# Kernel tuning notes

Measured on AMD Instinct MI355X. Metric: run time of the kernel, lower is better.

Reference implementation:

```python
import jax, jax.numpy as jnp
import numpy as np

N_NODES = 50000
N_EDGES = 800000
D_IN, D_HID, D_OUT = 96, 96, 48


def _gcn_conv(x, src, dst, W, b, num_nodes):
    """PyG GCNConv: h = x @ W; out[dst] += norm * h[src]; out += b.
    Symmetric normalization deg^{-1/2}[src] * deg^{-1/2}[dst], self-loops included
    (src/dst already contain self-loops)."""
    h = x @ W  # [N, d_out]
    deg = jax.ops.segment_sum(jnp.ones_like(dst, dtype=h.dtype), dst,
                              num_segments=num_nodes)  # in-degree incl. self-loop
    dinv = jnp.where(deg > 0, jax.lax.rsqrt(deg), 0.0)
    norm = dinv[src] * dinv[dst]  # [E+N]
    msgs = h[src] * norm[:, None]  # gather + scale (the memory-bound part)
    out = jax.ops.segment_sum(msgs, dst, num_segments=num_nodes)  # scatter-add
    return out + b


def setup_inputs() -> dict:
    key = jax.random.key(0)
    k1, k2, k3, k4 = jax.random.split(key, 4)
    x = jax.random.normal(k1, (N_NODES, D_IN), dtype=jnp.float32)
    edge_index = jax.random.randint(k2, (2, N_EDGES), 0, N_NODES, dtype=jnp.int64)
    # Glorot-ish init for weights, zero bias (matches GCNConv defaults)
    W1 = jax.random.normal(k3, (D_IN, D_HID), dtype=jnp.float32) / np.sqrt(D_IN)
    b1 = jnp.zeros((D_HID,), dtype=jnp.float32)
    W2 = jax.random.normal(k4, (D_HID, D_OUT), dtype=jnp.float32) / np.sqrt(D_HID)
    b2 = jnp.zeros((D_OUT,), dtype=jnp.float32)
    return {"x": x, "edge_index": edge_index, "W1": W1, "b1": b1, "W2": W2, "b2": b2}


def reference(x, edge_index, W1, b1, W2, b2):
    num_nodes = x.shape[0]
    loops = jnp.arange(num_nodes, dtype=edge_index.dtype)
    src = jnp.concatenate([edge_index[0], loops])  # add self-loops
    dst = jnp.concatenate([edge_index[1], loops])
    h = _gcn_conv(x, src, dst, W1, b1, num_nodes)
    h = jax.nn.relu(h)
    # dropout p=0.5 is identity in eval mode (self.training=False)
    out = _gcn_conv(h, src, dst, W2, b2, num_nodes)
    return out
```

## Files before the change

### kernel.cpp

```cpp
#include <hip/hip_runtime.h>
#include <hip/hip_bf16.h>


constexpr int NN = 50000;
constexpr int NE = 800000;
constexpr int DI = 96;
constexpr int DH = 96;
constexpr int DO = 48;

constexpr int BK_SHIFT = 6;
constexpr int NBK      = (NN + 63) >> 6;
constexpr int BK_CAP   = 2048;

constexpr int NCHUNK = 128;
constexpr int CH     = (NE + NCHUNK - 1) / NCHUNK;

typedef unsigned short ushort8 __attribute__((ext_vector_type(8)));

__device__ __forceinline__ float bf2f(unsigned short u) {
    return __uint_as_float(((unsigned int)u) << 16);
}
__device__ __forceinline__ unsigned short f2bf(float f) {
    __hip_bfloat16 b = __float2bfloat16(f);
    return *reinterpret_cast<unsigned short*>(&b);
}


__global__ __launch_bounds__(256) void k_hist(const int* __restrict__ dst,
                                              int* __restrict__ C, int e) {
    __shared__ int hist[NBK];
    for (int i = threadIdx.x; i < NBK; i += 256) hist[i] = 0;
    __syncthreads();
    const int blk = blockIdx.x;
    const int beg = blk * CH, end = min(beg + CH, e);
    for (int i = beg + threadIdx.x; i < end; i += 256)
        atomicAdd(&hist[dst[i] >> BK_SHIFT], 1);
    __syncthreads();
    for (int b = threadIdx.x; b < NBK; b += 256)
        C[b * NCHUNK + blk] = hist[b];
}

__global__ __launch_bounds__(256) void k_rowscan(int* __restrict__ C,
                                                 int* __restrict__ totals,
                                                 int* __restrict__ row_ptr) {
    if (blockIdx.x == 0 && threadIdx.x == 0) row_ptr[NN] = NE;
    const int w    = threadIdx.x >> 6;
    const int lane = threadIdx.x & 63;
    const int r    = blockIdx.x * 4 + w;
    if (r >= NBK) return;
    int* row = C + r * NCHUNK;
    const int v0 = row[lane];
    const int v1 = row[64 + lane];
    int s0 = v0, s1 = v1;
#pragma unroll
    for (int off = 1; off < 64; off <<= 1) {
        int y0 = __shfl_up(s0, off);
        int y1 = __shfl_up(s1, off);
        if (lane >= off) { s0 += y0; s1 += y1; }
    }
    s1 += __shfl(s0, 63);
    row[lane]      = s0 - v0;
    row[64 + lane] = s1 - v1;
    if (lane == 63) totals[r] = s1;
}

__global__ __launch_bounds__(256) void k_scatter(const int* __restrict__ src,
                                                 const int* __restrict__ dst,
                                                 const int* __restrict__ C,
                                                 const int* __restrict__ totals,
                                                 int* __restrict__ bk_ptr,
                                                 unsigned* __restrict__ ebuf, int e) {
    __shared__ int bkL[NBK + 1];
    __shared__ int part[256];
    __shared__ int cur[NBK];
    const int t = threadIdx.x;

    int v[4];
    int s = 0;
    const int base = t * 4;
#pragma unroll
    for (int i = 0; i < 4; ++i) {
        int idx = base + i;
        v[i] = (idx < NBK) ? totals[idx] : 0;
        s += v[i];
    }
    part[t] = s;
    __syncthreads();
#pragma unroll
    for (int off = 1; off < 256; off <<= 1) {
        int x = part[t];
        int a = (t >= off) ? part[t - off] : 0;
        __syncthreads();
        part[t] = x + a;
        __syncthreads();
    }
    int run = part[t] - s;
#pragma unroll
    for (int i = 0; i < 4; ++i) {
        int idx = base + i;
        if (idx <= NBK) bkL[idx] = run;
        run += v[i];
    }
    __syncthreads();

    const int blk = blockIdx.x;
    for (int b = t; b < NBK; b += 256) cur[b] = bkL[b] + C[b * NCHUNK + blk];
    if (blk == 0)
        for (int i = t; i <= NBK; i += 256) bk_ptr[i] = bkL[i];
    __syncthreads();

    const int beg = blk * CH, end = min(beg + CH, e);
    for (int i = beg + t; i < end; i += 256) {
        int d = dst[i];
        int b = d >> BK_SHIFT;
        int pos = atomicAdd(&cur[b], 1);
        ebuf[pos] = ((unsigned)(d & 63) << 16) | (unsigned)src[i];
    }
}

__global__ __launch_bounds__(256) void k_bsort(const unsigned* __restrict__ ebuf,
                                               const int* __restrict__ bk_ptr,
                                               int* __restrict__ row_ptr,
                                               float* __restrict__ dinv,
                                               int* __restrict__ src_sorted, int n) {
    __shared__ unsigned eL[BK_CAP];
    __shared__ int outL[BK_CAP];
    __shared__ int curL[64];
    __shared__ int baseL[64];

    const int b   = blockIdx.x;
    const int beg = bk_ptr[b];
    const int m   = bk_ptr[b + 1] - beg;
    const int t   = threadIdx.x;

    if (t < 64) curL[t] = 0;
    __syncthreads();

    for (int i = t; i < m; i += 256) {
        unsigned v = ebuf[beg + i];
        eL[i] = v;
        atomicAdd(&curL[v >> 16], 1);
    }
    __syncthreads();

    if (t < 64) {
        int c = curL[t];
        int x = c;
#pragma unroll
        for (int off = 1; off < 64; off <<= 1) {
            int y = __shfl_up(x, off);
            if (t >= off) x += y;
        }
        int excl = x - c;
        baseL[t] = excl;
        int d0 = (b << BK_SHIFT) + t;
        if (d0 < n) {
            row_ptr[d0] = beg + excl;
            dinv[d0]    = rsqrtf((float)(c + 1));
        }
    }
    __syncthreads();
    if (t < 64) curL[t] = baseL[t];
    __syncthreads();

    for (int i = t; i < m; i += 256) {
        unsigned v = eL[i];
        int p = atomicAdd(&curL[v >> 16], 1);
        outL[p] = (int)(v & 0xFFFFu);
    }
    __syncthreads();
    for (int i = t; i < m; i += 256) src_sorted[beg + i] = outL[i];
}


template<int DOUT, bool XBF16>
__global__ __launch_bounds__(256) void k_gemm(const void* __restrict__ Xin,
                                              const float* __restrict__ W,
                                              const float* __restrict__ dinv,
                                              unsigned short* __restrict__ H, int n) {
    constexpr int ROWS = 32;
    constexpr int CPT  = DOUT / 16;
    constexpr int RPT  = 2;

    __shared__ float ws[DI * DOUT];
    __shared__ unsigned char xraw[ROWS * DI * (XBF16 ? 2 : 4)];
    float*          xsf = reinterpret_cast<float*>(xraw);
    unsigned short* xsu = reinterpret_cast<unsigned short*>(xraw);

    const int tid  = threadIdx.x;
    const int row0 = blockIdx.x * ROWS;

    for (int i = tid; i < DI * DOUT; i += 256) ws[i] = W[i];

    if (XBF16) {
        const ushort8* Xv = reinterpret_cast<const ushort8*>(
            (const unsigned short*)Xin + (size_t)row0 * DI);
        ushort8* xv = reinterpret_cast<ushort8*>(xsu);
        const int nv   = ROWS * DI / 8;
        const int maxv = ((n - row0) * DI) / 8;
        for (int i = tid; i < nv; i += 256)
            xv[i] = (i < maxv) ? Xv[i] : (ushort8)(0);
    } else {
        const float4* Xv = reinterpret_cast<const float4*>(
            (const float*)Xin + (size_t)row0 * DI);
        float4* xv = reinterpret_cast<float4*>(xsf);
        const int nv   = ROWS * DI / 4;
        const int maxv = ((n - row0) * DI) / 4;
        for (int i = tid; i < nv; i += 256)
            xv[i] = (i < maxv) ? Xv[i] : float4{0.f, 0.f, 0.f, 0.f};
    }
    __syncthreads();

    const int cg = tid & 15;
    const int rg = tid >> 4;

    float acc[RPT][CPT];
#pragma unroll
    for (int i = 0; i < RPT; ++i)
#pragma unroll
        for (int j = 0; j < CPT; ++j) acc[i][j] = 0.f;

    for (int k = 0; k < DI; ++k) {
        float xv[RPT];
#pragma unroll
        for (int i = 0; i < RPT; ++i) {
            int r = rg * RPT + i;
            xv[i] = XBF16 ? bf2f(xsu[r * DI + k]) : xsf[r * DI + k];
        }
#pragma unroll
        for (int j = 0; j < CPT; ++j) {
            float wv = ws[k * DOUT + cg * CPT + j];
#pragma unroll
            for (int i = 0; i < RPT; ++i) acc[i][j] += xv[i] * wv;
        }
    }

#pragma unroll
    for (int i = 0; i < RPT; ++i) {
        int row = row0 + rg * RPT + i;
        if (row < n) {
            float dv = dinv[row];
#pragma unroll
            for (int j = 0; j < CPT; ++j)
                H[(size_t)row * DOUT + cg * CPT + j] = f2bf(acc[i][j] * dv);
        }
    }
}


template<int D, bool RELU, bool OUTBF16>
__global__ __launch_bounds__(256) void k_agg_csr(const unsigned short* __restrict__ h,
                                                 const float* __restrict__ dinv,
                                                 const int* __restrict__ row_ptr,
                                                 const int* __restrict__ src_sorted,
                                                 const float* __restrict__ bias,
                                                 void* __restrict__ outp, int n) {
    constexpr int G = D / 8;
    int t = blockIdx.x * blockDim.x + threadIdx.x;
    if (t >= n * G) return;
    const int node = t / G;
    const int g    = t % G;

    const ushort8* h8 = reinterpret_cast<const ushort8*>(h);

    float accA[8], accB[8];
    {
        ushort8 hv = h8[(size_t)node * G + g];
#pragma unroll
        for (int j = 0; j < 8; ++j) { accA[j] = bf2f(hv[j]); accB[j] = 0.f; }
    }

    const int beg = row_ptr[node];
    const int end = row_ptr[node + 1];
    int k = beg;
    int kA = min((beg + 3) & ~3, end);
    for (; k < kA; ++k) {
        int s = src_sorted[k];
        ushort8 vv = h8[(size_t)s * G + g];
#pragma unroll
        for (int j = 0; j < 8; ++j) accA[j] += bf2f(vv[j]);
    }
    const int4* sv = reinterpret_cast<const int4*>(src_sorted + k);
    for (; k + 4 <= end; k += 4) {
        int4 s4 = *sv++;
        ushort8 v0 = h8[(size_t)s4.x * G + g];
        ushort8 v1 = h8[(size_t)s4.y * G + g];
        ushort8 v2 = h8[(size_t)s4.z * G + g];
        ushort8 v3 = h8[(size_t)s4.w * G + g];
#pragma unroll
        for (int j = 0; j < 8; ++j) {
            accA[j] += bf2f(v0[j]) + bf2f(v1[j]);
            accB[j] += bf2f(v2[j]) + bf2f(v3[j]);
        }
    }
    for (; k < end; ++k) {
        int s = src_sorted[k];
        ushort8 vv = h8[(size_t)s * G + g];
#pragma unroll
        for (int j = 0; j < 8; ++j) accA[j] += bf2f(vv[j]);
    }

    const float di = dinv[node];
    const float4* b4 = reinterpret_cast<const float4*>(bias);
    float4 b0 = b4[g * 2], b1 = b4[g * 2 + 1];
    float r[8];
#pragma unroll
    for (int j = 0; j < 8; ++j) r[j] = di * (accA[j] + accB[j]);
    r[0] += b0.x; r[1] += b0.y; r[2] += b0.z; r[3] += b0.w;
    r[4] += b1.x; r[5] += b1.y; r[6] += b1.z; r[7] += b1.w;
    if (RELU) {
#pragma unroll
        for (int j = 0; j < 8; ++j) r[j] = fmaxf(r[j], 0.f);
    }
    if (OUTBF16) {
        ushort8 o;
#pragma unroll
        for (int j = 0; j < 8; ++j) o[j] = f2bf(r[j]);
        reinterpret_cast<ushort8*>((unsigned short*)outp)[(size_t)node * G + g] = o;
    } else {
        float4* o4 = reinterpret_cast<float4*>((float*)outp + (size_t)node * D + g * 8);
        o4[0] = float4{r[0], r[1], r[2], r[3]};
        o4[1] = float4{r[4], r[5], r[6], r[7]};
    }
}


extern "C" void kernel_launch(void* const* d_in, const int* in_sizes, int n_in,
                              void* d_out, int out_size, void* d_ws, size_t ws_size,
                              hipStream_t stream) {
    const float* x   = (const float*)d_in[0];
    const int*   ei  = (const int*)d_in[1];
    const float* W1  = (const float*)d_in[2];
    const float* b1  = (const float*)d_in[3];
    const float* W2  = (const float*)d_in[4];
    const float* b2  = (const float*)d_in[5];
    float*       out = (float*)d_out;

    const int* srcv = ei;
    const int* dstv = ei + NE;

    char* p = (char*)d_ws;
    float*          dinv  = (float*)p;           p += (size_t)NN * 4;
    unsigned short* a1    = (unsigned short*)p;  p += (size_t)NN * DH * 2;
    unsigned short* h1    = (unsigned short*)p;  p += (size_t)NN * DH * 2;
    int*      row_ptr     = (int*)p;             p += (size_t)(NN + 16) * 4;
    int*      src_sorted  = (int*)p;             p += (size_t)NE * 4;
    unsigned* ebuf        = (unsigned*)p;        p += (size_t)NE * 4;
    int*      Cm          = (int*)p;             p += (size_t)NBK * NCHUNK * 4;
    int*      totals      = (int*)p;             p += (size_t)NBK * 4;
    int*      bk_ptr      = (int*)p;             p += (size_t)(NBK + 1) * 4;

    const int B = 256;

    k_hist<<<NCHUNK, B, 0, stream>>>(dstv, Cm, NE);
    k_rowscan<<<(NBK + 3) / 4, B, 0, stream>>>(Cm, totals, row_ptr);
    k_scatter<<<NCHUNK, B, 0, stream>>>(srcv, dstv, Cm, totals, bk_ptr, ebuf, NE);
    k_bsort<<<NBK, B, 0, stream>>>(ebuf, bk_ptr, row_ptr, dinv, src_sorted, NN);

    k_gemm<DH, false><<<(NN + 31) / 32, B, 0, stream>>>(x, W1, dinv, h1, NN);
    {
        int total = NN * (DH / 8);
        k_agg_csr<DH, true, true><<<(total + B - 1) / B, B, 0, stream>>>(
            h1, dinv, row_ptr, src_sorted, b1, a1, NN);
    }

    unsigned short* h2 = h1;
    k_gemm<DO, true><<<(NN + 31) / 32, B, 0, stream>>>(a1, W2, dinv, h2, NN);
    {
        int total = NN * (DO / 8);
        k_agg_csr<DO, false, false><<<(total + B - 1) / B, B, 0, stream>>>(
            h2, dinv, row_ptr, src_sorted, b2, out, NN);
    }
}
```

Before: 127.3 us.

## Slice node features into per-slice arrays and shrink source indices to 16-bit

Node feature matrices are stored as 8 column slices, each a separate padded array (16 bf16 for layer 1, 8 for layer 2). The aggregation kernels now run one thread per node per slice, so all gathers within a block hit one slice, which is small enough to stay cache-resident. Sorted source indices are stored as 16-bit values, halving index traffic. The costs are padding bytes, less coalesced output writes, and 16-bit indices only fit because the node count is below 65536.

```diff
diff --git a/kernel.cpp b/kernel.cpp
--- a/kernel.cpp
+++ b/kernel.cpp
@@ -15,7 +15,8 @@
 constexpr int NCHUNK = 128;
 constexpr int CH     = (NE + NCHUNK - 1) / NCHUNK;
 
-typedef unsigned short ushort8 __attribute__((ext_vector_type(8)));
+typedef unsigned short us4 __attribute__((ext_vector_type(4)));
+typedef unsigned short us8 __attribute__((ext_vector_type(8)));
 
 __device__ __forceinline__ float bf2f(unsigned short u) {
     return __uint_as_float(((unsigned int)u) << 16);
@@ -122,9 +123,9 @@
                                                const int* __restrict__ bk_ptr,
                                                int* __restrict__ row_ptr,
                                                float* __restrict__ dinv,
-                                               int* __restrict__ src_sorted, int n) {
+                                               unsigned short* __restrict__ src16, int n) {
     __shared__ unsigned eL[BK_CAP];
-    __shared__ int outL[BK_CAP];
+    __shared__ unsigned short outL[BK_CAP];
     __shared__ int curL[64];
     __shared__ int baseL[64];
 
@@ -166,161 +167,241 @@
     for (int i = t; i < m; i += 256) {
         unsigned v = eL[i];
         int p = atomicAdd(&curL[v >> 16], 1);
-        outL[p] = (int)(v & 0xFFFFu);
-    }
-    __syncthreads();
-    for (int i = t; i < m; i += 256) src_sorted[beg + i] = outL[i];
-}
-
-
-template<int DOUT, bool XBF16>
-__global__ __launch_bounds__(256) void k_gemm(const void* __restrict__ Xin,
-                                              const float* __restrict__ W,
-                                              const float* __restrict__ dinv,
-                                              unsigned short* __restrict__ H, int n) {
-    constexpr int ROWS = 32;
-    constexpr int CPT  = DOUT / 16;
-    constexpr int RPT  = 2;
-
-    __shared__ float ws[DI * DOUT];
-    __shared__ unsigned char xraw[ROWS * DI * (XBF16 ? 2 : 4)];
-    float*          xsf = reinterpret_cast<float*>(xraw);
-    unsigned short* xsu = reinterpret_cast<unsigned short*>(xraw);
+        outL[p] = (unsigned short)(v & 0xFFFFu);
+    }
+    __syncthreads();
+    for (int i = t; i < m; i += 256) src16[beg + i] = outL[i];
+}
+
+
+__global__ __launch_bounds__(256) void k_gemm1(const float* __restrict__ X,
+                                               const float* __restrict__ W,
+                                               const float* __restrict__ dinv,
+                                               unsigned short* __restrict__ Hsl, int n) {
+    __shared__ float ws[DI * DH];
+    __shared__ float xs[32 * DI];
+    unsigned short* hout = reinterpret_cast<unsigned short*>(xs);
 
     const int tid  = threadIdx.x;
-    const int row0 = blockIdx.x * ROWS;
-
-    for (int i = tid; i < DI * DOUT; i += 256) ws[i] = W[i];
-
-    if (XBF16) {
-        const ushort8* Xv = reinterpret_cast<const ushort8*>(
-            (const unsigned short*)Xin + (size_t)row0 * DI);
-        ushort8* xv = reinterpret_cast<ushort8*>(xsu);
-        const int nv   = ROWS * DI / 8;
-        const int maxv = ((n - row0) * DI) / 8;
-        for (int i = tid; i < nv; i += 256)
-            xv[i] = (i < maxv) ? Xv[i] : (ushort8)(0);
-    } else {
-        const float4* Xv = reinterpret_cast<const float4*>(
-            (const float*)Xin + (size_t)row0 * DI);
-        float4* xv = reinterpret_cast<float4*>(xsf);
-        const int nv   = ROWS * DI / 4;
+    const int row0 = blockIdx.x * 32;
+
+    for (int i = tid; i < DI * DH; i += 256) ws[i] = W[i];
+    {
+        const float4* Xv = reinterpret_cast<const float4*>(X + (size_t)row0 * DI);
+        float4* xv = reinterpret_cast<float4*>(xs);
+        const int nv = 32 * DI / 4;
         const int maxv = ((n - row0) * DI) / 4;
         for (int i = tid; i < nv; i += 256)
             xv[i] = (i < maxv) ? Xv[i] : float4{0.f, 0.f, 0.f, 0.f};
     }
     __syncthreads();
 
-    const int cg = tid & 15;
-    const int rg = tid >> 4;
-
-    float acc[RPT][CPT];
-#pragma unroll
-    for (int i = 0; i < RPT; ++i)
-#pragma unroll
-        for (int j = 0; j < CPT; ++j) acc[i][j] = 0.f;
-
+    const int cg = tid & 15, rg = tid >> 4;
+    float acc[2][6] = {};
     for (int k = 0; k < DI; ++k) {
-        float xv[RPT];
-#pragma unroll
-        for (int i = 0; i < RPT; ++i) {
-            int r = rg * RPT + i;
-            xv[i] = XBF16 ? bf2f(xsu[r * DI + k]) : xsf[r * DI + k];
-        }
-#pragma unroll
-        for (int j = 0; j < CPT; ++j) {
-            float wv = ws[k * DOUT + cg * CPT + j];
-#pragma unroll
-            for (int i = 0; i < RPT; ++i) acc[i][j] += xv[i] * wv;
-        }
-    }
-
-#pragma unroll
-    for (int i = 0; i < RPT; ++i) {
-        int row = row0 + rg * RPT + i;
+        float x0 = xs[(rg * 2 + 0) * DI + k];
+        float x1 = xs[(rg * 2 + 1) * DI + k];
+#pragma unroll
+        for (int j = 0; j < 6; ++j) {
+            float wv = ws[k * DH + cg * 6 + j];
+            acc[0][j] += x0 * wv;
+            acc[1][j] += x1 * wv;
+        }
+    }
+    __syncthreads();
+
+#pragma unroll
+    for (int i = 0; i < 2; ++i) {
+        int row = row0 + rg * 2 + i;
+        float dv = (row < n) ? dinv[row] : 0.f;
+#pragma unroll
+        for (int j = 0; j < 6; ++j)
+            hout[(rg * 2 + i) * 96 + cg * 6 + j] = f2bf(acc[i][j] * dv);
+    }
+    __syncthreads();
+
+    {
+        int s = tid >> 5, r = tid & 31;
+        int row = row0 + r;
         if (row < n) {
-            float dv = dinv[row];
-#pragma unroll
-            for (int j = 0; j < CPT; ++j)
-                H[(size_t)row * DOUT + cg * CPT + j] = f2bf(acc[i][j] * dv);
-        }
-    }
-}
-
-
-template<int D, bool RELU, bool OUTBF16>
-__global__ __launch_bounds__(256) void k_agg_csr(const unsigned short* __restrict__ h,
-                                                 const float* __restrict__ dinv,
-                                                 const int* __restrict__ row_ptr,
-                                                 const int* __restrict__ src_sorted,
-                                                 const float* __restrict__ bias,
-                                                 void* __restrict__ outp, int n) {
-    constexpr int G = D / 8;
-    int t = blockIdx.x * blockDim.x + threadIdx.x;
-    if (t >= n * G) return;
-    const int node = t / G;
-    const int g    = t % G;
-
-    const ushort8* h8 = reinterpret_cast<const ushort8*>(h);
-
-    float accA[8], accB[8];
+            us8 lo, hi;
+#pragma unroll
+            for (int j = 0; j < 8; ++j) lo[j] = hout[r * 96 + s * 12 + j];
+#pragma unroll
+            for (int j = 0; j < 4; ++j) hi[j] = hout[r * 96 + s * 12 + 8 + j];
+#pragma unroll
+            for (int j = 4; j < 8; ++j) hi[j] = 0;
+            us8* dst = reinterpret_cast<us8*>(Hsl + ((size_t)s * n + row) * 16);
+            dst[0] = lo;
+            dst[1] = hi;
+        }
+    }
+}
+
+
+__global__ __launch_bounds__(256) void k_gemm2(const unsigned short* __restrict__ Asl,
+                                               const float* __restrict__ W,
+                                               const float* __restrict__ dinv,
+                                               unsigned short* __restrict__ Hsl, int n) {
+    __shared__ float ws[DH * DO];
+    __shared__ unsigned short xs[32 * DH];
+    const int tid  = threadIdx.x;
+    const int row0 = blockIdx.x * 32;
+
+    for (int i = tid; i < DH * DO; i += 256) ws[i] = W[i];
     {
-        ushort8 hv = h8[(size_t)node * G + g];
-#pragma unroll
-        for (int j = 0; j < 8; ++j) { accA[j] = bf2f(hv[j]); accB[j] = 0.f; }
+        int r = tid >> 3, s = tid & 7;
+        int row = row0 + r;
+        us4 a, b, c;
+        if (row < n) {
+            const us4* src = reinterpret_cast<const us4*>(Asl + ((size_t)s * n + row) * 16);
+            a = src[0]; b = src[1]; c = src[2];
+        } else {
+            a = (us4)(0); b = (us4)(0); c = (us4)(0);
+        }
+        us4* d = reinterpret_cast<us4*>(xs + r * DH + s * 12);
+        d[0] = a; d[1] = b; d[2] = c;
+    }
+    __syncthreads();
+
+    const int cg = tid & 15, rg = tid >> 4;
+    float acc[2][3] = {};
+    for (int k = 0; k < DH; ++k) {
+        float x0 = bf2f(xs[(rg * 2 + 0) * DH + k]);
+        float x1 = bf2f(xs[(rg * 2 + 1) * DH + k]);
+#pragma unroll
+        for (int j = 0; j < 3; ++j) {
+            float wv = ws[k * DO + cg * 3 + j];
+            acc[0][j] += x0 * wv;
+            acc[1][j] += x1 * wv;
+        }
+    }
+    __syncthreads();
+
+    unsigned short* hout = xs;
+#pragma unroll
+    for (int i = 0; i < 2; ++i) {
+        int row = row0 + rg * 2 + i;
+        float dv = (row < n) ? dinv[row] : 0.f;
+#pragma unroll
+        for (int j = 0; j < 3; ++j)
+            hout[(rg * 2 + i) * 48 + cg * 3 + j] = f2bf(acc[i][j] * dv);
+    }
+    __syncthreads();
+
+    {
+        int s = tid >> 5, r = tid & 31;
+        int row = row0 + r;
+        if (row < n) {
+            us8 v;
+#pragma unroll
+            for (int j = 0; j < 6; ++j) v[j] = hout[r * 48 + s * 6 + j];
+            v[6] = 0; v[7] = 0;
+            *reinterpret_cast<us8*>(Hsl + ((size_t)s * n + row) * 8) = v;
+        }
+    }
+}
+
+
+template<int SD, int RW, bool RELU, bool OUTSLICED>
+__global__ __launch_bounds__(256) void k_agg_sl(const unsigned short* __restrict__ hsl,
+                                                const float* __restrict__ dinv,
+                                                const int* __restrict__ row_ptr,
+                                                const unsigned short* __restrict__ src16,
+                                                const float* __restrict__ bias,
+                                                void* __restrict__ outp, int n) {
+    const int slice = blockIdx.x & 7;
+    const int node  = (blockIdx.x >> 3) * 256 + threadIdx.x;
+    if (node >= n) return;
+    const unsigned short* hs = hsl + (size_t)slice * n * RW;
+
+    float acc[SD];
+    if (SD == 12) {
+        const us8 lo = *reinterpret_cast<const us8*>(hs + (size_t)node * 16);
+        const us4 hi = *reinterpret_cast<const us4*>(hs + (size_t)node * 16 + 8);
+#pragma unroll
+        for (int j = 0; j < 8; ++j) acc[j] = bf2f(lo[j]);
+#pragma unroll
+        for (int j = 0; j < 4; ++j) acc[8 + j] = bf2f(hi[j]);
+    } else {
+        const us8 v = *reinterpret_cast<const us8*>(hs + (size_t)node * 8);
+#pragma unroll
+        for (int j = 0; j < SD; ++j) acc[j] = bf2f(v[j]);
     }
 
     const int beg = row_ptr[node];
     const int end = row_ptr[node + 1];
     int k = beg;
-    int kA = min((beg + 3) & ~3, end);
-    for (; k < kA; ++k) {
-        int s = src_sorted[k];
-        ushort8 vv = h8[(size_t)s * G + g];
-#pragma unroll
-        for (int j = 0; j < 8; ++j) accA[j] += bf2f(vv[j]);
-    }
-    const int4* sv = reinterpret_cast<const int4*>(src_sorted + k);
     for (; k + 4 <= end; k += 4) {
-        int4 s4 = *sv++;
-        ushort8 v0 = h8[(size_t)s4.x * G + g];
-        ushort8 v1 = h8[(size_t)s4.y * G + g];
-        ushort8 v2 = h8[(size_t)s4.z * G + g];
-        ushort8 v3 = h8[(size_t)s4.w * G + g];
-#pragma unroll
-        for (int j = 0; j < 8; ++j) {
-            accA[j] += bf2f(v0[j]) + bf2f(v1[j]);
-            accB[j] += bf2f(v2[j]) + bf2f(v3[j]);
+        int s0 = src16[k + 0];
+        int s1 = src16[k + 1];
+        int s2 = src16[k + 2];
+        int s3 = src16[k + 3];
+        if (SD == 12) {
+            const us8 a0 = *reinterpret_cast<const us8*>(hs + (size_t)s0 * 16);
+            const us8 a1 = *reinterpret_cast<const us8*>(hs + (size_t)s1 * 16);
+            const us8 a2 = *reinterpret_cast<const us8*>(hs + (size_t)s2 * 16);
+            const us8 a3 = *reinterpret_cast<const us8*>(hs + (size_t)s3 * 16);
+            const us4 b0 = *reinterpret_cast<const us4*>(hs + (size_t)s0 * 16 + 8);
+            const us4 b1 = *reinterpret_cast<const us4*>(hs + (size_t)s1 * 16 + 8);
+            const us4 b2 = *reinterpret_cast<const us4*>(hs + (size_t)s2 * 16 + 8);
+            const us4 b3 = *reinterpret_cast<const us4*>(hs + (size_t)s3 * 16 + 8);
+#pragma unroll
+            for (int j = 0; j < 8; ++j)
+                acc[j] += (bf2f(a0[j]) + bf2f(a1[j])) + (bf2f(a2[j]) + bf2f(a3[j]));
+#pragma unroll
+            for (int j = 0; j < 4; ++j)
+                acc[8 + j] += (bf2f(b0[j]) + bf2f(b1[j])) + (bf2f(b2[j]) + bf2f(b3[j]));
+        } else {
+            const us8 a0 = *reinterpret_cast<const us8*>(hs + (size_t)s0 * 8);
+            const us8 a1 = *reinterpret_cast<const us8*>(hs + (size_t)s1 * 8);
+            const us8 a2 = *reinterpret_cast<const us8*>(hs + (size_t)s2 * 8);
+            const us8 a3 = *reinterpret_cast<const us8*>(hs + (size_t)s3 * 8);
+#pragma unroll
+            for (int j = 0; j < SD; ++j)
+                acc[j] += (bf2f(a0[j]) + bf2f(a1[j])) + (bf2f(a2[j]) + bf2f(a3[j]));
         }
     }
     for (; k < end; ++k) {
-        int s = src_sorted[k];
-        ushort8 vv = h8[(size_t)s * G + g];
-#pragma unroll
-        for (int j = 0; j < 8; ++j) accA[j] += bf2f(vv[j]);
+        int s = src16[k];
+        if (SD == 12) {
+            const us8 a = *reinterpret_cast<const us8*>(hs + (size_t)s * 16);
+            const us4 b = *reinterpret_cast<const us4*>(hs + (size_t)s * 16 + 8);
+#pragma unroll
+            for (int j = 0; j < 8; ++j) acc[j] += bf2f(a[j]);
+#pragma unroll
+            for (int j = 0; j < 4; ++j) acc[8 + j] += bf2f(b[j]);
+        } else {
+            const us8 a = *reinterpret_cast<const us8*>(hs + (size_t)s * 8);
+#pragma unroll
+            for (int j = 0; j < SD; ++j) acc[j] += bf2f(a[j]);
+        }
     }
 
     const float di = dinv[node];
-    const float4* b4 = reinterpret_cast<const float4*>(bias);
-    float4 b0 = b4[g * 2], b1 = b4[g * 2 + 1];
-    float r[8];
-#pragma unroll
-    for (int j = 0; j < 8; ++j) r[j] = di * (accA[j] + accB[j]);
-    r[0] += b0.x; r[1] += b0.y; r[2] += b0.z; r[3] += b0.w;
-    r[4] += b1.x; r[5] += b1.y; r[6] += b1.z; r[7] += b1.w;
-    if (RELU) {
-#pragma unroll
-        for (int j = 0; j < 8; ++j) r[j] = fmaxf(r[j], 0.f);
-    }
-    if (OUTBF16) {
-        ushort8 o;
-#pragma unroll
-        for (int j = 0; j < 8; ++j) o[j] = f2bf(r[j]);
-        reinterpret_cast<ushort8*>((unsigned short*)outp)[(size_t)node * G + g] = o;
+    float r[SD];
+#pragma unroll
+    for (int j = 0; j < SD; ++j) {
+        r[j] = di * acc[j] + bias[slice * SD + j];
+        if (RELU) r[j] = fmaxf(r[j], 0.f);
+    }
+
+    if (OUTSLICED) {
+        unsigned short* o = (unsigned short*)outp + ((size_t)slice * n + node) * 16;
+        us8 lo;
+        us4 hi;
+#pragma unroll
+        for (int j = 0; j < 8; ++j) lo[j] = f2bf(r[j]);
+#pragma unroll
+        for (int j = 0; j < 4; ++j) hi[j] = f2bf(r[8 + j]);
+        *reinterpret_cast<us8*>(o) = lo;
+        *reinterpret_cast<us4*>(o + 8) = hi;
+        *reinterpret_cast<us4*>(o + 12) = (us4)(0);
     } else {
-        float4* o4 = reinterpret_cast<float4*>((float*)outp + (size_t)node * D + g * 8);
-        o4[0] = float4{r[0], r[1], r[2], r[3]};
-        o4[1] = float4{r[4], r[5], r[6], r[7]};
+        float* o = (float*)outp + (size_t)node * DO + slice * SD;
+#pragma unroll
+        for (int j = 0; j < SD / 2; ++j)
+            *reinterpret_cast<float2*>(o + j * 2) = float2{r[j * 2], r[j * 2 + 1]};
     }
 }
 
@@ -341,34 +422,29 @@
 
     char* p = (char*)d_ws;
     float*          dinv  = (float*)p;           p += (size_t)NN * 4;
-    unsigned short* a1    = (unsigned short*)p;  p += (size_t)NN * DH * 2;
-    unsigned short* h1    = (unsigned short*)p;  p += (size_t)NN * DH * 2;
+    unsigned short* a1sl  = (unsigned short*)p;  p += (size_t)8 * NN * 16 * 2;
+    unsigned short* h1sl  = (unsigned short*)p;  p += (size_t)8 * NN * 16 * 2;
     int*      row_ptr     = (int*)p;             p += (size_t)(NN + 16) * 4;
-    int*      src_sorted  = (int*)p;             p += (size_t)NE * 4;
+    unsigned short* src16 = (unsigned short*)p;  p += (size_t)NE * 2;
     unsigned* ebuf        = (unsigned*)p;        p += (size_t)NE * 4;
     int*      Cm          = (int*)p;             p += (size_t)NBK * NCHUNK * 4;
     int*      totals      = (int*)p;             p += (size_t)NBK * 4;
     int*      bk_ptr      = (int*)p;             p += (size_t)(NBK + 1) * 4;
 
     const int B = 256;
+    const int NCH_NODES = (NN + 255) / 256;
 
     k_hist<<<NCHUNK, B, 0, stream>>>(dstv, Cm, NE);
     k_rowscan<<<(NBK + 3) / 4, B, 0, stream>>>(Cm, totals, row_ptr);
     k_scatter<<<NCHUNK, B, 0, stream>>>(srcv, dstv, Cm, totals, bk_ptr, ebuf, NE);
-    k_bsort<<<NBK, B, 0, stream>>>(ebuf, bk_ptr, row_ptr, dinv, src_sorted, NN);
-
-    k_gemm<DH, false><<<(NN + 31) / 32, B, 0, stream>>>(x, W1, dinv, h1, NN);
-    {
-        int total = NN * (DH / 8);
-        k_agg_csr<DH, true, true><<<(total + B - 1) / B, B, 0, stream>>>(
-            h1, dinv, row_ptr, src_sorted, b1, a1, NN);
-    }
-
-    unsigned short* h2 = h1;
-    k_gemm<DO, true><<<(NN + 31) / 32, B, 0, stream>>>(a1, W2, dinv, h2, NN);
-    {
-        int total = NN * (DO / 8);
-        k_agg_csr<DO, false, false><<<(total + B - 1) / B, B, 0, stream>>>(
-            h2, dinv, row_ptr, src_sorted, b2, out, NN);
-    }
-}
+    k_bsort<<<NBK, B, 0, stream>>>(ebuf, bk_ptr, row_ptr, dinv, src16, NN);
+
+    k_gemm1<<<(NN + 31) / 32, B, 0, stream>>>(x, W1, dinv, h1sl, NN);
+    k_agg_sl<12, 16, true, true><<<NCH_NODES * 8, B, 0, stream>>>(
+        h1sl, dinv, row_ptr, src16, b1, a1sl, NN);
+
+    unsigned short* h2sl = h1sl;
+    k_gemm2<<<(NN + 31) / 32, B, 0, stream>>>(a1sl, W2, dinv, h2sl, NN);
+    k_agg_sl<6, 8, false, false><<<NCH_NODES * 8, B, 0, stream>>>(
+        h2sl, dinv, row_ptr, src16, b2, out, NN);
+}
```

Measured after the change: 177.9 us. 39.7% more time.

## Store sorted sources as 16-bit indices, unroll gather by 8, widen histogram chunks

Applied to the files above, without the earlier changes.

Sorted source indices are now stored as unsigned 16-bit values instead of 32-bit ints. This halves index traffic in both aggregation kernels and lets each 16-byte load bring in 8 indices, so the gather loop is unrolled to 8 outstanding row loads. The edge histogram and scatter use 256 chunks instead of 128, and the row scan handles four 64-wide segments per row. The 16-bit encoding only works while node ids fit below 65536, which holds for this node count but also applies to the existing packed ebuf format.

```diff
diff --git a/kernel.cpp b/kernel.cpp
--- a/kernel.cpp
+++ b/kernel.cpp
@@ -12,10 +12,10 @@
 constexpr int NBK      = (NN + 63) >> 6;
 constexpr int BK_CAP   = 2048;
 
-constexpr int NCHUNK = 128;
+constexpr int NCHUNK = 256;
 constexpr int CH     = (NE + NCHUNK - 1) / NCHUNK;
 
-typedef unsigned short ushort8 __attribute__((ext_vector_type(8)));
+typedef unsigned short us8 __attribute__((ext_vector_type(8)));
 
 __device__ __forceinline__ float bf2f(unsigned short u) {
     return __uint_as_float(((unsigned int)u) << 16);
@@ -49,19 +49,26 @@
     const int r    = blockIdx.x * 4 + w;
     if (r >= NBK) return;
     int* row = C + r * NCHUNK;
-    const int v0 = row[lane];
-    const int v1 = row[64 + lane];
-    int s0 = v0, s1 = v1;
+    int v[4], s[4];
+#pragma unroll
+    for (int q = 0; q < 4; ++q) { v[q] = row[q * 64 + lane]; s[q] = v[q]; }
 #pragma unroll
     for (int off = 1; off < 64; off <<= 1) {
-        int y0 = __shfl_up(s0, off);
-        int y1 = __shfl_up(s1, off);
-        if (lane >= off) { s0 += y0; s1 += y1; }
-    }
-    s1 += __shfl(s0, 63);
-    row[lane]      = s0 - v0;
-    row[64 + lane] = s1 - v1;
-    if (lane == 63) totals[r] = s1;
+#pragma unroll
+        for (int q = 0; q < 4; ++q) {
+            int y = __shfl_up(s[q], off);
+            if (lane >= off) s[q] += y;
+        }
+    }
+    int c0 = __shfl(s[0], 63);
+    int c1 = __shfl(s[1], 63);
+    int c2 = __shfl(s[2], 63);
+    s[1] += c0;
+    s[2] += c0 + c1;
+    s[3] += c0 + c1 + c2;
+#pragma unroll
+    for (int q = 0; q < 4; ++q) row[q * 64 + lane] = s[q] - v[q];
+    if (lane == 63) totals[r] = s[3];
 }
 
 __global__ __launch_bounds__(256) void k_scatter(const int* __restrict__ src,
@@ -122,9 +129,9 @@
                                                const int* __restrict__ bk_ptr,
                                                int* __restrict__ row_ptr,
                                                float* __restrict__ dinv,
-                                               int* __restrict__ src_sorted, int n) {
+                                               unsigned short* __restrict__ src16, int n) {
     __shared__ unsigned eL[BK_CAP];
-    __shared__ int outL[BK_CAP];
+    __shared__ unsigned short outL[BK_CAP];
     __shared__ int curL[64];
     __shared__ int baseL[64];
 
@@ -166,10 +173,10 @@
     for (int i = t; i < m; i += 256) {
         unsigned v = eL[i];
         int p = atomicAdd(&curL[v >> 16], 1);
-        outL[p] = (int)(v & 0xFFFFu);
-    }
-    __syncthreads();
-    for (int i = t; i < m; i += 256) src_sorted[beg + i] = outL[i];
+        outL[p] = (unsigned short)(v & 0xFFFFu);
+    }
+    __syncthreads();
+    for (int i = t; i < m; i += 256) src16[beg + i] = outL[i];
 }
 
 
@@ -193,13 +200,13 @@
     for (int i = tid; i < DI * DOUT; i += 256) ws[i] = W[i];
 
     if (XBF16) {
-        const ushort8* Xv = reinterpret_cast<const ushort8*>(
+        const us8* Xv = reinterpret_cast<const us8*>(
             (const unsigned short*)Xin + (size_t)row0 * DI);
-        ushort8* xv = reinterpret_cast<ushort8*>(xsu);
+        us8* xv = reinterpret_cast<us8*>(xsu);
         const int nv   = ROWS * DI / 8;
         const int maxv = ((n - row0) * DI) / 8;
         for (int i = tid; i < nv; i += 256)
-            xv[i] = (i < maxv) ? Xv[i] : (ushort8)(0);
+            xv[i] = (i < maxv) ? Xv[i] : (us8)(0);
     } else {
         const float4* Xv = reinterpret_cast<const float4*>(
             (const float*)Xin + (size_t)row0 * DI);
@@ -252,7 +259,7 @@
 __global__ __launch_bounds__(256) void k_agg_csr(const unsigned short* __restrict__ h,
                                                  const float* __restrict__ dinv,
                                                  const int* __restrict__ row_ptr,
-                                                 const int* __restrict__ src_sorted,
+                                                 const unsigned short* __restrict__ src16,
                                                  const float* __restrict__ bias,
                                                  void* __restrict__ outp, int n) {
     constexpr int G = D / 8;
@@ -261,11 +268,11 @@
     const int node = t / G;
     const int g    = t % G;
 
-    const ushort8* h8 = reinterpret_cast<const ushort8*>(h);
+    const us8* h8 = reinterpret_cast<const us8*>(h);
 
     float accA[8], accB[8];
     {
-        ushort8 hv = h8[(size_t)node * G + g];
+        us8 hv = h8[(size_t)node * G + g];
 #pragma unroll
         for (int j = 0; j < 8; ++j) { accA[j] = bf2f(hv[j]); accB[j] = 0.f; }
     }
@@ -273,31 +280,32 @@
     const int beg = row_ptr[node];
     const int end = row_ptr[node + 1];
     int k = beg;
-    int kA = min((beg + 3) & ~3, end);
+    int kA = min((beg + 7) & ~7, end);
     for (; k < kA; ++k) {
-        int s = src_sorted[k];
-        ushort8 vv = h8[(size_t)s * G + g];
+        us8 vv = h8[(size_t)src16[k] * G + g];
 #pragma unroll
         for (int j = 0; j < 8; ++j) accA[j] += bf2f(vv[j]);
     }
-    const int4* sv = reinterpret_cast<const int4*>(src_sorted + k);
-    for (; k + 4 <= end; k += 4) {
-        int4 s4 = *sv++;
-        ushort8 v0 = h8[(size_t)s4.x * G + g];
-        ushort8 v1 = h8[(size_t)s4.y * G + g];
-        ushort8 v2 = h8[(size_t)s4.z * G + g];
-        ushort8 v3 = h8[(size_t)s4.w * G + g];
+    for (; k + 8 <= end; k += 8) {
+        us8 si = *reinterpret_cast<const us8*>(src16 + k);
+        us8 v0 = h8[(size_t)si[0] * G + g];
+        us8 v1 = h8[(size_t)si[1] * G + g];
+        us8 v2 = h8[(size_t)si[2] * G + g];
+        us8 v3 = h8[(size_t)si[3] * G + g];
+        us8 v4 = h8[(size_t)si[4] * G + g];
+        us8 v5 = h8[(size_t)si[5] * G + g];
+        us8 v6 = h8[(size_t)si[6] * G + g];
+        us8 v7 = h8[(size_t)si[7] * G + g];
 #pragma unroll
         for (int j = 0; j < 8; ++j) {
-            accA[j] += bf2f(v0[j]) + bf2f(v1[j]);
-            accB[j] += bf2f(v2[j]) + bf2f(v3[j]);
+            accA[j] += (bf2f(v0[j]) + bf2f(v1[j])) + (bf2f(v4[j]) + bf2f(v5[j]));
+            accB[j] += (bf2f(v2[j]) + bf2f(v3[j])) + (bf2f(v6[j]) + bf2f(v7[j]));
         }
     }
     for (; k < end; ++k) {
-        int s = src_sorted[k];
-        ushort8 vv = h8[(size_t)s * G + g];
-#pragma unroll
-        for (int j = 0; j < 8; ++j) accA[j] += bf2f(vv[j]);
+        us8 vv = h8[(size_t)src16[k] * G + g];
+#pragma unroll
+        for (int j = 0; j < 8; ++j) accB[j] += bf2f(vv[j]);
     }
 
     const float di = dinv[node];
@@ -313,10 +321,10 @@
         for (int j = 0; j < 8; ++j) r[j] = fmaxf(r[j], 0.f);
     }
     if (OUTBF16) {
-        ushort8 o;
+        us8 o;
 #pragma unroll
         for (int j = 0; j < 8; ++j) o[j] = f2bf(r[j]);
-        reinterpret_cast<ushort8*>((unsigned short*)outp)[(size_t)node * G + g] = o;
+        reinterpret_cast<us8*>((unsigned short*)outp)[(size_t)node * G + g] = o;
     } else {
         float4* o4 = reinterpret_cast<float4*>((float*)outp + (size_t)node * D + g * 8);
         o4[0] = float4{r[0], r[1], r[2], r[3]};
@@ -344,7 +352,7 @@
     unsigned short* a1    = (unsigned short*)p;  p += (size_t)NN * DH * 2;
     unsigned short* h1    = (unsigned short*)p;  p += (size_t)NN * DH * 2;
     int*      row_ptr     = (int*)p;             p += (size_t)(NN + 16) * 4;
-    int*      src_sorted  = (int*)p;             p += (size_t)NE * 4;
+    unsigned short* src16 = (unsigned short*)p;  p += (size_t)NE * 2;
     unsigned* ebuf        = (unsigned*)p;        p += (size_t)NE * 4;
     int*      Cm          = (int*)p;             p += (size_t)NBK * NCHUNK * 4;
     int*      totals      = (int*)p;             p += (size_t)NBK * 4;
@@ -355,13 +363,13 @@
     k_hist<<<NCHUNK, B, 0, stream>>>(dstv, Cm, NE);
     k_rowscan<<<(NBK + 3) / 4, B, 0, stream>>>(Cm, totals, row_ptr);
     k_scatter<<<NCHUNK, B, 0, stream>>>(srcv, dstv, Cm, totals, bk_ptr, ebuf, NE);
-    k_bsort<<<NBK, B, 0, stream>>>(ebuf, bk_ptr, row_ptr, dinv, src_sorted, NN);
+    k_bsort<<<NBK, B, 0, stream>>>(ebuf, bk_ptr, row_ptr, dinv, src16, NN);
 
     k_gemm<DH, false><<<(NN + 31) / 32, B, 0, stream>>>(x, W1, dinv, h1, NN);
     {
         int total = NN * (DH / 8);
         k_agg_csr<DH, true, true><<<(total + B - 1) / B, B, 0, stream>>>(
-            h1, dinv, row_ptr, src_sorted, b1, a1, NN);
+            h1, dinv, row_ptr, src16, b1, a1, NN);
     }
 
     unsigned short* h2 = h1;
@@ -369,6 +377,6 @@
     {
         int total = NN * (DO / 8);
         k_agg_csr<DO, false, false><<<(total + B - 1) / B, B, 0, stream>>>(
-            h2, dinv, row_ptr, src_sorted, b2, out, NN);
-    }
-}
+            h2, dinv, row_ptr, src16, b2, out, NN);
+    }
+}
```

Measured after the change: 123.9 us. 2.7% less time.
